# Performance work log

Hardware: AMD Instinct MI355X
Metric: run time of the kernel (lower is better)

The kernel has to match this reference:

```python
import jax, jax.numpy as jnp
import numpy as np

NUM_GRAPHS = 1024


def setup_inputs() -> dict:
    key = jax.random.key(0)
    k1, k2, k3, k4 = jax.random.split(key, 4)
    N, D = 1000000, 128
    node_embeddings = jax.random.normal(k1, (N, D), dtype=jnp.float32)
    batch_idx = jnp.sort(jax.random.randint(k2, (N,), 0, NUM_GRAPHS))
    # gate MLP params (Linear(D,D) -> ReLU -> Linear(D,1)), scaled like kaiming-ish init
    W1 = jax.random.normal(k3, (D, D), dtype=jnp.float32) / np.sqrt(D)
    b1 = jnp.zeros((D,), dtype=jnp.float32)
    W2 = jax.random.normal(k4, (D, 1), dtype=jnp.float32) / np.sqrt(D)
    b2 = jnp.zeros((1,), dtype=jnp.float32)
    return {"node_embeddings": node_embeddings, "batch_idx": batch_idx,
            "W1": W1, "b1": b1, "W2": W2, "b2": b2}


def reference(node_embeddings, batch_idx, W1, b1, W2, b2):
    # gate = sigmoid(Linear(ReLU(Linear(x))))  -> [N, 1]
    h = jax.nn.relu(node_embeddings @ W1 + b1)          # [N, D]
    gate = jax.nn.sigmoid(h @ W2 + b2)                   # [N, 1]
    gated = gate * node_embeddings                       # [N, D]
    # scatter-sum over batch_idx -> per-graph embedding [B, D]
    graph_embedding = jax.ops.segment_sum(gated, batch_idx, num_segments=NUM_GRAPHS)
    return graph_embedding
```

## Files before the change

### kernel.cpp

```cpp
#include <hip/hip_runtime.h>
#include <stdint.h>

#define D 128
#define TM 64
#define GRID 512
#define NTHREADS 256

typedef float f32x4 __attribute__((ext_vector_type(4)));
typedef short s16x8 __attribute__((ext_vector_type(8)));
typedef uint32_t u32x2 __attribute__((ext_vector_type(2)));

__device__ __forceinline__ uint32_t f2bf_u(float f) {
    union { float f; uint32_t u; } v; v.f = f;
    return (v.u + 0x7fffu + ((v.u >> 16) & 1u)) >> 16;
}
__device__ __forceinline__ short f2bf(float f) { return (short)f2bf_u(f); }
__device__ __forceinline__ uint32_t cvt_pk_bf16(float lo, float hi) {
    uint32_t r;
    asm("v_cvt_pk_bf16_f32 %0, %1, %2" : "=v"(r) : "v"(lo), "v"(hi));
    return r;
}

__global__ __launch_bounds__(NTHREADS, 2)
void gate_agg_kernel(const float* __restrict__ X,
                     const int* __restrict__ bidx,
                     const float* __restrict__ W1,
                     const float* __restrict__ b1,
                     const float* __restrict__ W2,
                     const float* __restrict__ b2,
                     float* __restrict__ out,
                     int NT)
{
    __shared__ short w1p[16 * D * 8];
    __shared__ short xt[2][TM * D];
    __shared__ u32x2 gidW[TM];

    const int tid = threadIdx.x;
    const int l = tid & 63;
    const int w = tid >> 6;
    const int l15 = l & 15;
    const int lk = l >> 4;

    for (int i = tid; i < D * D; i += NTHREADS) {
        int k = i >> 7, n = i & 127;
        w1p[(((k >> 3) * D) + n) * 8 + (k & 7)] = f2bf(W1[i]);
    }
    float b1v[8], w2v[8];
    #pragma unroll
    for (int ct = 0; ct < 8; ++ct) {
        b1v[ct] = b1[ct * 16 + l15];
        w2v[ct] = W2[ct * 16 + l15];
    }
    const float b2s = b2[0];

    const int q = NT / GRID, rem = NT % GRID;
    int t0, t1;
    if ((int)blockIdx.x < rem) { t0 = blockIdx.x * (q + 1); t1 = t0 + q + 1; }
    else { t0 = rem * (q + 1) + ((int)blockIdx.x - rem) * q; t1 = t0 + q; }

    float acc3[2] = {0.f, 0.f};
    int cur = -1;

    f32x4 vA[8], vB[8];
    int ridxA = 0, ridxB = 0;
    if (t0 < t1) {
        const float* xg = X + (size_t)t0 * TM * D;
        #pragma unroll
        for (int j = 0; j < 8; ++j) vA[j] = *(const f32x4*)(xg + (size_t)(j * 256 + tid) * 4);
        if (l < 16) ridxA = bidx[(size_t)t0 * TM + 16 * w + l];
    }
    if (t0 + 1 < t1) {
        const float* xg = X + (size_t)(t0 + 1) * TM * D;
        #pragma unroll
        for (int j = 0; j < 8; ++j) vB[j] = *(const f32x4*)(xg + (size_t)(j * 256 + tid) * 4);
        if (l < 16) ridxB = bidx[(size_t)(t0 + 1) * TM + 16 * w + l];
    }

    asm volatile("s_waitcnt lgkmcnt(0)" ::: "memory");
    __builtin_amdgcn_s_barrier();

#define BODY(V, RIDX, PB)                                                        \
    {                                                                            \
               \
        _Pragma("unroll")                                                        \
        for (int j = 0; j < 8; ++j) {                                            \
            int qc = j * 256 + tid;                                              \
            int row = qc >> 5, cq = qc & 31;                                     \
            int c2 = cq >> 1, h = cq & 1;                                        \
            u32x2 wv;                                                            \
            wv[0] = cvt_pk_bf16(V[j][0], V[j][1]);                               \
            wv[1] = cvt_pk_bf16(V[j][2], V[j][3]);                               \
            *(u32x2*)((char*)xt[PB] + row * 256 + ((c2 ^ (row & 15)) << 4) + h * 8) = wv; \
        }                                                                        \
        const int ridx_cur = RIDX;                                               \
                           \
        if (t + 2 < t1) {                                                        \
            const float* xg = X + (size_t)(t + 2) * TM * D;                      \
            _Pragma("unroll")                                                    \
            for (int j = 0; j < 8; ++j)                                          \
                V[j] = *(const f32x4*)(xg + (size_t)(j * 256 + tid) * 4);        \
            if (l < 16) RIDX = bidx[(size_t)(t + 2) * TM + 16 * w + l];          \
        }                                                                        \
        asm volatile("s_waitcnt lgkmcnt(0)" ::: "memory");                       \
        __builtin_amdgcn_s_barrier();                                            \
        __builtin_amdgcn_sched_barrier(0);                                       \
                                   \
        f32x4 acc[8];                                                            \
        _Pragma("unroll")                                                        \
        for (int ct = 0; ct < 8; ++ct) acc[ct] = (f32x4)0.f;                     \
        {                                                                        \
            const int R = 16 * w + l15;                                          \
            const char* rb = (const char*)xt[PB] + R * 256;                      \
            _Pragma("unroll")                                                    \
            for (int kt = 0; kt < 4; ++kt) {                                     \
                const int kc = kt * 4 + lk;                                      \
                s16x8 a = *(const s16x8*)(rb + ((kc ^ l15) << 4));               \
                _Pragma("unroll")                                                \
                for (int ct = 0; ct < 8; ++ct) {                                 \
                    s16x8 bf = *(const s16x8*)&w1p[(kc * D + ct * 16 + l15) * 8];\
                    acc[ct] = __builtin_amdgcn_mfma_f32_16x16x32_bf16(a, bf, acc[ct], 0, 0, 0); \
                }                                                                \
            }                                                                    \
        }                                                                        \
               \
        {                                                                        \
            float p[4] = {0.f, 0.f, 0.f, 0.f};                                   \
            _Pragma("unroll")                                                    \
            for (int ct = 0; ct < 8; ++ct) {                                     \
                _Pragma("unroll")                                                \
                for (int r = 0; r < 4; ++r) {                                    \
                    float h = acc[ct][r] + b1v[ct];                              \
                    h = fmaxf(h, 0.f);                                           \
                    p[r] = fmaf(h, w2v[ct], p[r]);                               \
                }                                                                \
            }                                                                    \
            _Pragma("unroll")                                                    \
            for (int r = 0; r < 4; ++r) {                                        \
                p[r] += __shfl_xor(p[r], 1, 64);                                 \
                p[r] += __shfl_xor(p[r], 2, 64);                                 \
                p[r] += __shfl_xor(p[r], 4, 64);                                 \
                p[r] += __shfl_xor(p[r], 8, 64);                                 \
            }                                                                    \
            const int sel = l15;                                                 \
            float ps = p[0];                                                     \
            ps = (sel == 1) ? p[1] : ps;                                         \
            ps = (sel == 2) ? p[2] : ps;                                         \
            ps = (sel == 3) ? p[3] : ps;                                         \
            const int rr = lk * 4 + sel;             \
            const int seg = __shfl(ridx_cur, rr & 15, 64);                       \
            if (sel < 4) {                                                       \
                float g = 1.f / (1.f + __expf(-(ps + b2s)));                     \
                u32x2 gi; gi[0] = __float_as_uint(g); gi[1] = (uint32_t)seg;     \
                gidW[16 * w + rr] = gi;                                          \
            }                                                                    \
        }                                                                        \
                      \
        _Pragma("unroll")                                                        \
        for (int r = 0; r < 16; ++r) {                                           \
            u32x2 gi = gidW[16 * w + r];                                         \
            const int seg = (int)gi[1];                                          \
            const float g = __uint_as_float(gi[0]);                              \
            if (seg != cur) {                                                    \
                if (cur >= 0) {                                                  \
                    atomicAdd(out + (size_t)cur * D + 2 * l,     acc3[0]);       \
                    atomicAdd(out + (size_t)cur * D + 2 * l + 1, acc3[1]);       \
                }                                                                \
                acc3[0] = 0.f; acc3[1] = 0.f; cur = seg;                         \
            }                                                                    \
            const int Rr = 16 * w + r;                                           \
            uint32_t xw = *(const uint32_t*)((const char*)xt[PB] + Rr * 256 +    \
                           ((((l >> 2) ^ (Rr & 15)) << 4)) + (l & 3) * 4);       \
            acc3[0] = fmaf(g, __uint_as_float(xw << 16),          acc3[0]);      \
            acc3[1] = fmaf(g, __uint_as_float(xw & 0xffff0000u),  acc3[1]);      \
        }                                                                        \
    }

    int t = t0;
    while (t < t1) {
        BODY(vA, ridxA, 0);
        ++t; if (t >= t1) break;
        BODY(vB, ridxB, 1);
        ++t;
    }
#undef BODY

    if (cur >= 0) {
        atomicAdd(out + (size_t)cur * D + 2 * l,     acc3[0]);
        atomicAdd(out + (size_t)cur * D + 2 * l + 1, acc3[1]);
    }
}

extern "C" void kernel_launch(void* const* d_in, const int* in_sizes, int n_in,
                              void* d_out, int out_size, void* d_ws, size_t ws_size,
                              hipStream_t stream) {
    const float* X    = (const float*)d_in[0];
    const int*   bidx = (const int*)d_in[1];
    const float* W1   = (const float*)d_in[2];
    const float* b1   = (const float*)d_in[3];
    const float* W2   = (const float*)d_in[4];
    const float* b2   = (const float*)d_in[5];
    float* out = (float*)d_out;

    const int N  = in_sizes[0] / D;
    const int NT = N / TM;

    hipMemsetAsync(d_out, 0, (size_t)out_size * sizeof(float), stream);
    gate_agg_kernel<<<GRID, NTHREADS, 0, stream>>>(X, bidx, W1, b1, W2, b2, out, NT);
}
```

Before: 113.8 us.

## Keep W1 fragments in registers and split hidden columns across eight waves

The block grows to 512 threads, and each wave now holds a 16-column slice of W1 as bf16 MFMA fragments in registers. This removes the 32 KB W1 copy in LDS and the per-iteration LDS reads of W1. Each wave runs MFMAs over all 64 rows of the tile for its slice, and the per-node gate partials are reduced across waves through a small padded LDS buffer. The cost is an extra block-wide barrier per tile plus a cross-wave reduction step, and each wave now handles only 8 rows in the segment-sum phase.

```diff
diff --git a/kernel.cpp b/kernel.cpp
--- a/kernel.cpp
+++ b/kernel.cpp
@@ -4,17 +4,17 @@
 #define D 128
 #define TM 64
 #define GRID 512
-#define NTHREADS 256
+#define NTHREADS 512
+#define PPW 9
 
 typedef float f32x4 __attribute__((ext_vector_type(4)));
 typedef short s16x8 __attribute__((ext_vector_type(8)));
 typedef uint32_t u32x2 __attribute__((ext_vector_type(2)));
 
-__device__ __forceinline__ uint32_t f2bf_u(float f) {
+__device__ __forceinline__ short f2bf(float f) {
     union { float f; uint32_t u; } v; v.f = f;
-    return (v.u + 0x7fffu + ((v.u >> 16) & 1u)) >> 16;
-}
-__device__ __forceinline__ short f2bf(float f) { return (short)f2bf_u(f); }
+    return (short)((v.u + 0x7fffu + ((v.u >> 16) & 1u)) >> 16);
+}
 __device__ __forceinline__ uint32_t cvt_pk_bf16(float lo, float hi) {
     uint32_t r;
     asm("v_cvt_pk_bf16_f32 %0, %1, %2" : "=v"(r) : "v"(lo), "v"(hi));
@@ -31,9 +31,9 @@
                      float* __restrict__ out,
                      int NT)
 {
-    __shared__ short w1p[16 * D * 8];
     __shared__ short xt[2][TM * D];
-    __shared__ u32x2 gidW[TM];
+    __shared__ float pp[64 * PPW];
+    __shared__ u32x2 gid[TM];
 
     const int tid = threadIdx.x;
     const int l = tid & 63;
@@ -41,15 +41,18 @@
     const int l15 = l & 15;
     const int lk = l >> 4;
 
-    for (int i = tid; i < D * D; i += NTHREADS) {
-        int k = i >> 7, n = i & 127;
-        w1p[(((k >> 3) * D) + n) * 8 + (k & 7)] = f2bf(W1[i]);
-    }
-    float b1v[8], w2v[8];
+    s16x8 bfr[4];
     #pragma unroll
-    for (int ct = 0; ct < 8; ++ct) {
-        b1v[ct] = b1[ct * 16 + l15];
-        w2v[ct] = W2[ct * 16 + l15];
+    for (int kt = 0; kt < 4; ++kt)
+        #pragma unroll
+        for (int e = 0; e < 8; ++e)
+            bfr[kt][e] = f2bf(W1[(kt * 32 + lk * 8 + e) * D + 16 * w + l15]);
+
+    float b1v[4], w2v[4];
+    #pragma unroll
+    for (int r = 0; r < 4; ++r) {
+        b1v[r] = b1[16 * w + lk * 4 + r];
+        w2v[r] = W2[16 * w + lk * 4 + r];
     }
     const float b2s = b2[0];
 
@@ -61,30 +64,27 @@
     float acc3[2] = {0.f, 0.f};
     int cur = -1;
 
-    f32x4 vA[8], vB[8];
+    f32x4 vA[4], vB[4];
     int ridxA = 0, ridxB = 0;
     if (t0 < t1) {
         const float* xg = X + (size_t)t0 * TM * D;
         #pragma unroll
-        for (int j = 0; j < 8; ++j) vA[j] = *(const f32x4*)(xg + (size_t)(j * 256 + tid) * 4);
-        if (l < 16) ridxA = bidx[(size_t)t0 * TM + 16 * w + l];
+        for (int j = 0; j < 4; ++j) vA[j] = *(const f32x4*)(xg + (size_t)(j * 512 + tid) * 4);
+        if (l < 8) ridxA = bidx[(size_t)t0 * TM + 8 * w + l];
     }
     if (t0 + 1 < t1) {
         const float* xg = X + (size_t)(t0 + 1) * TM * D;
         #pragma unroll
-        for (int j = 0; j < 8; ++j) vB[j] = *(const f32x4*)(xg + (size_t)(j * 256 + tid) * 4);
-        if (l < 16) ridxB = bidx[(size_t)(t0 + 1) * TM + 16 * w + l];
-    }
-
-    asm volatile("s_waitcnt lgkmcnt(0)" ::: "memory");
-    __builtin_amdgcn_s_barrier();
+        for (int j = 0; j < 4; ++j) vB[j] = *(const f32x4*)(xg + (size_t)(j * 512 + tid) * 4);
+        if (l < 8) ridxB = bidx[(size_t)(t0 + 1) * TM + 8 * w + l];
+    }
 
 #define BODY(V, RIDX, PB)                                                        \
     {                                                                            \
-               \
-        _Pragma("unroll")                                                        \
-        for (int j = 0; j < 8; ++j) {                                            \
-            int qc = j * 256 + tid;                                              \
+             \
+        _Pragma("unroll")                                                        \
+        for (int j = 0; j < 4; ++j) {                                            \
+            int qc = j * 512 + tid;                                              \
             int row = qc >> 5, cq = qc & 31;                                     \
             int c2 = cq >> 1, h = cq & 1;                                        \
             u32x2 wv;                                                            \
@@ -93,71 +93,65 @@
             *(u32x2*)((char*)xt[PB] + row * 256 + ((c2 ^ (row & 15)) << 4) + h * 8) = wv; \
         }                                                                        \
         const int ridx_cur = RIDX;                                               \
-                           \
+          \
         if (t + 2 < t1) {                                                        \
             const float* xg = X + (size_t)(t + 2) * TM * D;                      \
             _Pragma("unroll")                                                    \
-            for (int j = 0; j < 8; ++j)                                          \
-                V[j] = *(const f32x4*)(xg + (size_t)(j * 256 + tid) * 4);        \
-            if (l < 16) RIDX = bidx[(size_t)(t + 2) * TM + 16 * w + l];          \
+            for (int j = 0; j < 4; ++j)                                          \
+                V[j] = *(const f32x4*)(xg + (size_t)(j * 512 + tid) * 4);        \
+            if (l < 8) RIDX = bidx[(size_t)(t + 2) * TM + 8 * w + l];            \
         }                                                                        \
         asm volatile("s_waitcnt lgkmcnt(0)" ::: "memory");                       \
-        __builtin_amdgcn_s_barrier();                                            \
+        __builtin_amdgcn_s_barrier();                               \
         __builtin_amdgcn_sched_barrier(0);                                       \
-                                   \
-        f32x4 acc[8];                                                            \
-        _Pragma("unroll")                                                        \
-        for (int ct = 0; ct < 8; ++ct) acc[ct] = (f32x4)0.f;                     \
-        {                                                                        \
-            const int R = 16 * w + l15;                                          \
-            const char* rb = (const char*)xt[PB] + R * 256;                      \
-            _Pragma("unroll")                                                    \
-            for (int kt = 0; kt < 4; ++kt) {                                     \
-                const int kc = kt * 4 + lk;                                      \
-                s16x8 a = *(const s16x8*)(rb + ((kc ^ l15) << 4));               \
-                _Pragma("unroll")                                                \
-                for (int ct = 0; ct < 8; ++ct) {                                 \
-                    s16x8 bf = *(const s16x8*)&w1p[(kc * D + ct * 16 + l15) * 8];\
-                    acc[ct] = __builtin_amdgcn_mfma_f32_16x16x32_bf16(a, bf, acc[ct], 0, 0, 0); \
-                }                                                                \
+                \
+        f32x4 acc[4];                                                            \
+        acc[0] = (f32x4)0.f; acc[1] = (f32x4)0.f;                                \
+        acc[2] = (f32x4)0.f; acc[3] = (f32x4)0.f;                                \
+        _Pragma("unroll")                                                        \
+        for (int kt = 0; kt < 4; ++kt) {                                         \
+            const int kc = kt * 4 + lk;                                          \
+            _Pragma("unroll")                                                    \
+            for (int nf = 0; nf < 4; ++nf) {                                     \
+                const int R = nf * 16 + l15;                                     \
+                s16x8 xb = *(const s16x8*)((const char*)xt[PB] + R * 256 + ((kc ^ l15) << 4)); \
+                acc[nf] = __builtin_amdgcn_mfma_f32_16x16x32_bf16(bfr[kt], xb, acc[nf], 0, 0, 0); \
             }                                                                    \
         }                                                                        \
-               \
-        {                                                                        \
-            float p[4] = {0.f, 0.f, 0.f, 0.f};                                   \
-            _Pragma("unroll")                                                    \
-            for (int ct = 0; ct < 8; ++ct) {                                     \
-                _Pragma("unroll")                                                \
-                for (int r = 0; r < 4; ++r) {                                    \
-                    float h = acc[ct][r] + b1v[ct];                              \
-                    h = fmaxf(h, 0.f);                                           \
-                    p[r] = fmaf(h, w2v[ct], p[r]);                               \
-                }                                                                \
+          \
+        _Pragma("unroll")                                                        \
+        for (int nf = 0; nf < 4; ++nf) {                                         \
+            float s = 0.f;                                                       \
+            _Pragma("unroll")                                                    \
+            for (int r = 0; r < 4; ++r) {                                        \
+                float h = acc[nf][r] + b1v[r];                                   \
+                h = fmaxf(h, 0.f);                                               \
+                s = fmaf(h, w2v[r], s);                                          \
             }                                                                    \
-            _Pragma("unroll")                                                    \
-            for (int r = 0; r < 4; ++r) {                                        \
-                p[r] += __shfl_xor(p[r], 1, 64);                                 \
-                p[r] += __shfl_xor(p[r], 2, 64);                                 \
-                p[r] += __shfl_xor(p[r], 4, 64);                                 \
-                p[r] += __shfl_xor(p[r], 8, 64);                                 \
-            }                                                                    \
-            const int sel = l15;                                                 \
-            float ps = p[0];                                                     \
-            ps = (sel == 1) ? p[1] : ps;                                         \
-            ps = (sel == 2) ? p[2] : ps;                                         \
-            ps = (sel == 3) ? p[3] : ps;                                         \
-            const int rr = lk * 4 + sel;             \
-            const int seg = __shfl(ridx_cur, rr & 15, 64);                       \
-            if (sel < 4) {                                                       \
-                float g = 1.f / (1.f + __expf(-(ps + b2s)));                     \
-                u32x2 gi; gi[0] = __float_as_uint(g); gi[1] = (uint32_t)seg;     \
-                gidW[16 * w + rr] = gi;                                          \
-            }                                                                    \
-        }                                                                        \
-                      \
-        _Pragma("unroll")                                                        \
-        for (int r = 0; r < 16; ++r) {                                           \
-            u32x2 gi = gidW[16 * w + r];                                         \
+            s += __shfl_xor(s, 16, 64);                                          \
+            s += __shfl_xor(s, 32, 64);                                          \
+            if (l < 16) pp[(nf * 16 + l) * PPW + w] = s;                         \
+        }                                                                        \
+        asm volatile("s_waitcnt lgkmcnt(0)" ::: "memory");                       \
+        __builtin_amdgcn_s_barrier();                                  \
+        __builtin_amdgcn_sched_barrier(0);                                       \
+         \
+        if (l < 8) {                                                             \
+            const int node = 8 * w + l;                                          \
+            float s = 0.f;                                                       \
+            _Pragma("unroll")                                                    \
+            for (int c = 0; c < 8; ++c) s += pp[node * PPW + c];                 \
+            float g = 1.f / (1.f + __expf(-(s + b2s)));                          \
+            u32x2 gi; gi[0] = __float_as_uint(g); gi[1] = (uint32_t)ridx_cur;    \
+            gid[node] = gi;                                                      \
+        }                                                                        \
+        asm volatile("s_waitcnt lgkmcnt(0)" ::: "memory");    \
+        __builtin_amdgcn_sched_barrier(0);                                       \
+           \
+        _Pragma("unroll")                                                        \
+        for (int r = 0; r < 8; ++r) {                                            \
+            const int row = 8 * w + r;                                           \
+            u32x2 gi = gid[row];                                                 \
             const int seg = (int)gi[1];                                          \
             const float g = __uint_as_float(gi[0]);                              \
             if (seg != cur) {                                                    \
@@ -167,11 +161,10 @@
                 }                                                                \
                 acc3[0] = 0.f; acc3[1] = 0.f; cur = seg;                         \
             }                                                                    \
-            const int Rr = 16 * w + r;                                           \
-            uint32_t xw = *(const uint32_t*)((const char*)xt[PB] + Rr * 256 +    \
-                           ((((l >> 2) ^ (Rr & 15)) << 4)) + (l & 3) * 4);       \
-            acc3[0] = fmaf(g, __uint_as_float(xw << 16),          acc3[0]);      \
-            acc3[1] = fmaf(g, __uint_as_float(xw & 0xffff0000u),  acc3[1]);      \
+            uint32_t xv = *(const uint32_t*)((const char*)xt[PB] + row * 256 +   \
+                           ((((l >> 2) ^ (row & 15)) << 4)) + (l & 3) * 4);      \
+            acc3[0] = fmaf(g, __uint_as_float(xv << 16),         acc3[0]);       \
+            acc3[1] = fmaf(g, __uint_as_float(xv & 0xffff0000u), acc3[1]);       \
         }                                                                        \
     }
 
```

Result: faster. 110.7 us (median of 2 runs) (-2.8%).
